# Performance work log

Measured on AMD Instinct MI355X. Metric: run time of the kernel, lower is better.

## Reference

```python
import jax, jax.numpy as jnp
import numpy as np

D_MODEL, H, D_K = 768, 12, 64
B, S = 2, 2048
NEG = -1.0e9


def setup_inputs() -> dict:
    key = jax.random.key(0)
    ks = jax.random.split(key, 7)
    q = jax.random.normal(ks[0], (B, S, D_MODEL), dtype=jnp.float32)
    k = jax.random.normal(ks[1], (B, S, D_MODEL), dtype=jnp.float32)
    v = jax.random.normal(ks[2], (B, S, D_MODEL), dtype=jnp.float32)
    mask = jnp.tril(jnp.ones((S, S), dtype=jnp.int32))[None, None]  # [1,1,S,S] causal
    sc = 1.0 / np.sqrt(D_MODEL)
    w_q = jax.random.normal(ks[3], (D_MODEL, D_MODEL), dtype=jnp.float32) * sc
    w_k = jax.random.normal(ks[4], (D_MODEL, D_MODEL), dtype=jnp.float32) * sc
    w_v = jax.random.normal(ks[5], (D_MODEL, D_MODEL), dtype=jnp.float32) * sc
    w_o = jax.random.normal(ks[6], (D_MODEL, D_MODEL), dtype=jnp.float32) * sc
    return {"q": q, "k": k, "v": v, "mask": mask,
            "w_q": w_q, "w_k": w_k, "w_v": w_v, "w_o": w_o}


def reference(q, k, v, mask, w_q, w_k, w_v, w_o):
    # nn.Linear(x) = x @ W.T ; split heads: [B,S,D] -> [B,H,S,Dk]
    def split_heads(x, w):
        y = jnp.einsum('bsd,ed->bse', x, w)
        return y.reshape(x.shape[0], x.shape[1], H, D_K).transpose(0, 2, 1, 3)

    qh = split_heads(q, w_q)
    kh = split_heads(k, w_k)
    vh = split_heads(v, w_v)
    scores = jnp.einsum('bhqd,bhkd->bhqk', qh, kh) / jnp.sqrt(jnp.float32(D_K))
    scores = jnp.where(mask == 0, jnp.float32(NEG), scores)
    attn = jax.nn.softmax(scores, axis=-1)  # dropout p=0 -> identity
    ctx = jnp.einsum('bhqk,bhkd->bhqd', attn, vh)
    ctx = ctx.transpose(0, 2, 1, 3).reshape(q.shape[0], q.shape[1], D_MODEL)
    return jnp.einsum('bsd,ed->bse', ctx, w_o)
```

## Files before the change

kernel.cpp:

```cpp
#include <hip/hip_runtime.h>

#define DM   768
#define HN   12
#define DKH  64
#define BSZ  2
#define SEQ  2048
#define MROWS (BSZ*SEQ)
#define NEGBIG -1.0e9f

typedef __bf16 bf16;
typedef __bf16 bf16x8 __attribute__((ext_vector_type(8)));
typedef __bf16 bf16x4 __attribute__((ext_vector_type(4)));
typedef float  f32x4  __attribute__((ext_vector_type(4)));
typedef unsigned int uint32;

__device__ __forceinline__ void gload_lds16(const void* g, void* l) {
    __builtin_amdgcn_global_load_lds(
        (const __attribute__((address_space(1))) char*)g,
        (__attribute__((address_space(3))) char*)l, 16, 0, 0);
}

__global__ __launch_bounds__(256) void cvt3(const float* __restrict__ a, const float* __restrict__ b,
                                            const float* __restrict__ c,
                                            bf16* __restrict__ x, bf16* __restrict__ y,
                                            bf16* __restrict__ z, int n) {
    const float* s; bf16* d;
    if      (blockIdx.y == 0) { s = a; d = x; }
    else if (blockIdx.y == 1) { s = b; d = y; }
    else                      { s = c; d = z; }
    int i = (blockIdx.x * 256 + threadIdx.x) * 4;
    if (i + 3 < n) {
        float4 v = *(const float4*)(s + i);
        bf16x4 o; o[0] = (bf16)v.x; o[1] = (bf16)v.y; o[2] = (bf16)v.z; o[3] = (bf16)v.w;
        *(bf16x4*)(d + i) = o;
    }
}
__global__ __launch_bounds__(256) void cvt4(const float* __restrict__ a, const float* __restrict__ b,
                                            const float* __restrict__ c, const float* __restrict__ e,
                                            bf16* __restrict__ x, bf16* __restrict__ y,
                                            bf16* __restrict__ z, bf16* __restrict__ u, int n) {
    const float* s; bf16* d;
    if      (blockIdx.y == 0) { s = a; d = x; }
    else if (blockIdx.y == 1) { s = b; d = y; }
    else if (blockIdx.y == 2) { s = c; d = z; }
    else                      { s = e; d = u; }
    int i = (blockIdx.x * 256 + threadIdx.x) * 4;
    if (i + 3 < n) {
        float4 v = *(const float4*)(s + i);
        bf16x4 o; o[0] = (bf16)v.x; o[1] = (bf16)v.y; o[2] = (bf16)v.z; o[3] = (bf16)v.w;
        *(bf16x4*)(d + i) = o;
    }
}

__global__ __launch_bounds__(256) void gemm_qkv(
    const bf16* __restrict__ xq, const bf16* __restrict__ xk, const bf16* __restrict__ xv,
    const bf16* __restrict__ wq, const bf16* __restrict__ wk, const bf16* __restrict__ wv,
    bf16* __restrict__ qh, bf16* __restrict__ kh, bf16* __restrict__ vt)
{
    __shared__ bf16 As[128 * 32];
    __shared__ bf16 Bs[128 * 32];

    const bf16* A; const bf16* Bw; bf16* Out;
    if      (blockIdx.z == 0) { A = xq; Bw = wq; Out = qh; }
    else if (blockIdx.z == 1) { A = xk; Bw = wk; Out = kh; }
    else                      { A = xv; Bw = wv; Out = vt; }
    const bool vout = (blockIdx.z == 2);

    const int t = threadIdx.x, w = t >> 6, lane = t & 63;
    const int mt = blockIdx.x * 128, nt = blockIdx.y * 128;
    const int wr = (w >> 1) * 64, wc = (w & 1) * 64;

    f32x4 acc[4][4] = {};

    for (int k0 = 0; k0 < DM; k0 += 32) {
        #pragma unroll
        for (int i = 0; i < 2; i++) {
            int c = i * 256 + t;
            int row = c >> 2, col = (c & 3) * 8;
            gload_lds16(A  + (size_t)(mt + row) * DM + k0 + col, (char*)As + c * 16);
            gload_lds16(Bw + (size_t)(nt + row) * DM + k0 + col, (char*)Bs + c * 16);
        }
        asm volatile("s_waitcnt vmcnt(0)" ::: "memory");
        __syncthreads();

        bf16x8 af[4], bfr[4];
        #pragma unroll
        for (int m = 0; m < 4; m++)
            af[m] = *(const bf16x8*)&As[(wr + m * 16 + (lane & 15)) * 32 + (lane >> 4) * 8];
        #pragma unroll
        for (int n = 0; n < 4; n++)
            bfr[n] = *(const bf16x8*)&Bs[(wc + n * 16 + (lane & 15)) * 32 + (lane >> 4) * 8];
        #pragma unroll
        for (int m = 0; m < 4; m++)
            #pragma unroll
            for (int n = 0; n < 4; n++)
                acc[m][n] = __builtin_amdgcn_mfma_f32_16x16x32_bf16(af[m], bfr[n], acc[m][n], 0, 0, 0);
        __syncthreads();
    }

    if (!vout) {
        #pragma unroll
        for (int m = 0; m < 4; m++) {
            #pragma unroll
            for (int n = 0; n < 4; n++) {
                #pragma unroll
                for (int r = 0; r < 4; r++) {
                    int gm = mt + wr + m * 16 + (lane >> 4) * 4 + r;
                    int gn = nt + wc + n * 16 + (lane & 15);
                    int b = gm >> 11, s = gm & 2047, h = gn >> 6, d = gn & 63;
                    Out[(((size_t)b * HN + h) * SEQ + s) * DKH + d] = (bf16)acc[m][n][r];
                }
            }
        }
    } else {
        #pragma unroll
        for (int m = 0; m < 4; m++) {
            #pragma unroll
            for (int n = 0; n < 4; n++) {
                int gm = mt + wr + m * 16 + (lane >> 4) * 4;
                int gn = nt + wc + n * 16 + (lane & 15);
                int b = gm >> 11, s0 = gm & 2047, h = gn >> 6, d = gn & 63;
                bf16x4 pk;
                #pragma unroll
                for (int r = 0; r < 4; r++) pk[r] = (bf16)acc[m][n][r];
                *(bf16x4*)&Out[(((size_t)b * HN + h) * DKH + d) * SEQ + s0] = pk;
            }
        }
    }
}

__global__ __launch_bounds__(256) void gemm_out(
    const bf16* __restrict__ Actx, const bf16* __restrict__ Bw, float* __restrict__ Out)
{
    __shared__ bf16 As[128 * 32];
    __shared__ bf16 Bs[128 * 32];

    const int t = threadIdx.x, w = t >> 6, lane = t & 63;
    const int mt = blockIdx.x * 128, nt = blockIdx.y * 128;
    const int wr = (w >> 1) * 64, wc = (w & 1) * 64;

    f32x4 acc[4][4] = {};

    for (int k0 = 0; k0 < DM; k0 += 32) {
        #pragma unroll
        for (int i = 0; i < 2; i++) {
            int c = i * 256 + t;
            int row = c >> 2, col = (c & 3) * 8;
            gload_lds16(Actx + (size_t)(mt + row) * DM + k0 + col, (char*)As + c * 16);
            gload_lds16(Bw   + (size_t)(nt + row) * DM + k0 + col, (char*)Bs + c * 16);
        }
        asm volatile("s_waitcnt vmcnt(0)" ::: "memory");
        __syncthreads();

        bf16x8 af[4], bfr[4];
        #pragma unroll
        for (int m = 0; m < 4; m++)
            af[m] = *(const bf16x8*)&As[(wr + m * 16 + (lane & 15)) * 32 + (lane >> 4) * 8];
        #pragma unroll
        for (int n = 0; n < 4; n++)
            bfr[n] = *(const bf16x8*)&Bs[(wc + n * 16 + (lane & 15)) * 32 + (lane >> 4) * 8];
        #pragma unroll
        for (int m = 0; m < 4; m++)
            #pragma unroll
            for (int n = 0; n < 4; n++)
                acc[m][n] = __builtin_amdgcn_mfma_f32_16x16x32_bf16(af[m], bfr[n], acc[m][n], 0, 0, 0);
        __syncthreads();
    }

    #pragma unroll
    for (int m = 0; m < 4; m++) {
        #pragma unroll
        for (int n = 0; n < 4; n++) {
            #pragma unroll
            for (int r = 0; r < 4; r++) {
                int gm = mt + wr + m * 16 + (lane >> 4) * 4 + r;
                int gn = nt + wc + n * 16 + (lane & 15);
                Out[(size_t)gm * DM + gn] = acc[m][n][r];
            }
        }
    }
}

__global__ __launch_bounds__(256) void flash_attn(
    const bf16* __restrict__ qh, const bf16* __restrict__ kh,
    const bf16* __restrict__ vt, bf16* __restrict__ ctx)
{
    __shared__ bf16 Ks[2][4096];
    __shared__ bf16 Vs[2][4096];
    __shared__ bf16 pl[4][16 * 72];

    const int qt = (blockIdx.x & 1) ? (31 - (blockIdx.x >> 1)) : (int)(blockIdx.x >> 1);
    const int qb = qt * 64;
    const int bh = blockIdx.y;
    const int t = threadIdx.x, w = t >> 6, lane = t & 63;
    const int g = lane >> 4, lo = lane & 15;
    const size_t base = (size_t)bh * SEQ * DKH;
    const char* khead = (const char*)(kh + base);
    const char* vhead = (const char*)(vt + base);

    uint32 koff[2], voff[2];
    #pragma unroll
    for (int i = 0; i < 2; i++) {
        int c = w * 128 + i * 64 + lane;
        int r = c >> 3, s = c & 7;
        int sw = s ^ (r & 7);
        koff[i] = (uint32)(r * 128  + 16 * sw);
        voff[i] = (uint32)(r * 4096 + 16 * sw);
    }
    const uint32 kr0 = (uint32)(128 * lo + 16 * (g ^ (lo & 7)));
    const uint32 kr1 = kr0 ^ 64;

    const bf16* qp = qh + base + (size_t)(qb + w * 16 + lo) * DKH + g * 8;
    bf16x8 q0 = *(const bf16x8*)qp;
    bf16x8 q1 = *(const bf16x8*)(qp + 32);

    f32x4 O[4] = {};
    float m_old = -1e30f, l_run = 0.0f;
    const int qrow = qb + w * 16 + lo;
    bf16* plw = &pl[w][0];

    const int T = qt + 1;

    #pragma unroll
    for (int i = 0; i < 2; i++) {
        int c16 = (w * 128 + i * 64 + lane) * 16;
        gload_lds16(khead + koff[i], (char*)&Ks[0][0] + c16);
        gload_lds16(vhead + voff[i], (char*)&Vs[0][0] + c16);
    }
    asm volatile("s_waitcnt vmcnt(0)" ::: "memory");
    __syncthreads();

    for (int it = 0; it < T; ++it) {
        const int par = it & 1, nxt = par ^ 1;
        if (it + 1 < T) {
            const char* ks = khead + (size_t)(it + 1) * 8192;
            const char* vs = vhead + (size_t)(it + 1) * 128;
            #pragma unroll
            for (int i = 0; i < 2; i++) {
                int c16 = (w * 128 + i * 64 + lane) * 16;
                gload_lds16(ks + koff[i], (char*)&Ks[nxt][0] + c16);
                gload_lds16(vs + voff[i], (char*)&Vs[nxt][0] + c16);
            }
        }

        const char* Kp = (const char*)&Ks[par][0];
        f32x4 s[4];
        __builtin_amdgcn_s_setprio(1);
        #pragma unroll
        for (int cg = 0; cg < 4; cg++) {
            bf16x8 kf0 = *(const bf16x8*)(Kp + cg * 2048 + kr0);
            bf16x8 kf1 = *(const bf16x8*)(Kp + cg * 2048 + kr1);
            f32x4 z = {0.0f, 0.0f, 0.0f, 0.0f};
            z = __builtin_amdgcn_mfma_f32_16x16x32_bf16(kf0, q0, z, 0, 0, 0);
            z = __builtin_amdgcn_mfma_f32_16x16x32_bf16(kf1, q1, z, 0, 0, 0);
            s[cg] = z;
        }
        __builtin_amdgcn_s_setprio(0);

        if (it == T - 1) {
            #pragma unroll
            for (int cg = 0; cg < 4; cg++)
                #pragma unroll
                for (int r = 0; r < 4; r++) {
                    int ki = it * 64 + cg * 16 + 4 * g + r;
                    float v = s[cg][r] * 0.125f;
                    s[cg][r] = (ki > qrow) ? NEGBIG : v;
                }
        } else {
            #pragma unroll
            for (int cg = 0; cg < 4; cg++)
                #pragma unroll
                for (int r = 0; r < 4; r++) s[cg][r] *= 0.125f;
        }

        float mx = fmaxf(fmaxf(fmaxf(s[0][0], s[0][1]), fmaxf(s[0][2], s[0][3])),
                         fmaxf(fmaxf(s[1][0], s[1][1]), fmaxf(s[1][2], s[1][3])));
        mx = fmaxf(mx, fmaxf(fmaxf(fmaxf(s[2][0], s[2][1]), fmaxf(s[2][2], s[2][3])),
                             fmaxf(fmaxf(s[3][0], s[3][1]), fmaxf(s[3][2], s[3][3]))));
        mx = fmaxf(mx, __shfl_xor(mx, 16, 64));
        mx = fmaxf(mx, __shfl_xor(mx, 32, 64));

        float mnew = fmaxf(m_old, mx);
        float scl  = __expf(m_old - mnew);
        m_old = mnew;
        float rs = 0.0f;
        #pragma unroll
        for (int cg = 0; cg < 4; cg++)
            #pragma unroll
            for (int r = 0; r < 4; r++) {
                s[cg][r] = __expf(s[cg][r] - mnew);
                rs += s[cg][r];
            }
        rs += __shfl_xor(rs, 16, 64);
        rs += __shfl_xor(rs, 32, 64);
        l_run = l_run * scl + rs;

        float scl4[4];
        #pragma unroll
        for (int r = 0; r < 4; r++) scl4[r] = __shfl(scl, 4 * g + r, 64);
        #pragma unroll
        for (int dg = 0; dg < 4; dg++)
            #pragma unroll
            for (int r = 0; r < 4; r++) O[dg][r] *= scl4[r];

        #pragma unroll
        for (int cg = 0; cg < 4; cg++) {
            bf16x4 pk;
            #pragma unroll
            for (int r = 0; r < 4; r++) pk[r] = (bf16)s[cg][r];
            *(bf16x4*)&plw[lo * 72 + cg * 16 + 4 * g] = pk;
        }
        asm volatile("s_waitcnt lgkmcnt(0)" ::: "memory");
        __builtin_amdgcn_sched_barrier(0);

        const char* Vp = (const char*)&Vs[par][0];
        __builtin_amdgcn_s_setprio(1);
        #pragma unroll
        for (int kq = 0; kq < 2; kq++) {
            bf16x8 pa = *(const bf16x8*)&plw[lo * 72 + kq * 32 + 8 * g];
            #pragma unroll
            for (int dblk = 0; dblk < 4; dblk++) {
                int row = dblk * 16 + lo;
                bf16x8 vv = *(const bf16x8*)(Vp + row * 128 + 16 * ((4 * kq + g) ^ (lo & 7)));
                O[dblk] = __builtin_amdgcn_mfma_f32_16x16x32_bf16(pa, vv, O[dblk], 0, 0, 0);
            }
        }
        __builtin_amdgcn_s_setprio(0);

        asm volatile("s_waitcnt vmcnt(0)" ::: "memory");
        __syncthreads();
    }

    float inv4[4];
    #pragma unroll
    for (int r = 0; r < 4; r++) inv4[r] = 1.0f / __shfl(l_run, 4 * g + r, 64);
    const int b = bh / HN, h = bh % HN;
    #pragma unroll
    for (int dg = 0; dg < 4; dg++) {
        #pragma unroll
        for (int r = 0; r < 4; r++) {
            int row = qb + w * 16 + g * 4 + r;
            ctx[((size_t)(b * SEQ + row)) * DM + h * DKH + dg * 16 + lo] =
                (bf16)(O[dg][r] * inv4[r]);
        }
    }
}

extern "C" void kernel_launch(void* const* d_in, const int* in_sizes, int n_in,
                              void* d_out, int out_size, void* d_ws, size_t ws_size,
                              hipStream_t stream) {
    const float* q  = (const float*)d_in[0];
    const float* k  = (const float*)d_in[1];
    const float* v  = (const float*)d_in[2];
    const float* wq = (const float*)d_in[4];
    const float* wk = (const float*)d_in[5];
    const float* wv = (const float*)d_in[6];
    const float* wo = (const float*)d_in[7];
    float* out = (float*)d_out;

    const size_t NX = (size_t)MROWS * DM;
    const size_t NW = (size_t)DM * DM;

    bf16* p = (bf16*)d_ws;
    bf16* xq  = p; p += NX;
    bf16* xk  = p; p += NX;
    bf16* xv  = p; p += NX;
    bf16* wqb = p; p += NW;
    bf16* wkb = p; p += NW;
    bf16* wvb = p; p += NW;
    bf16* wob = p; p += NW;
    bf16* qhp = p; p += NX;
    bf16* khp = p; p += NX;
    bf16* vtp = p; p += NX;
    bf16* ctxp = p; p += NX;

    cvt3<<<dim3(NX / 1024, 3), 256, 0, stream>>>(q, k, v, xq, xk, xv, (int)NX);
    cvt4<<<dim3(NW / 1024, 4), 256, 0, stream>>>(wq, wk, wv, wo, wqb, wkb, wvb, wob, (int)NW);

    gemm_qkv<<<dim3(MROWS / 128, DM / 128, 3), 256, 0, stream>>>(
        xq, xk, xv, wqb, wkb, wvb, qhp, khp, vtp);

    flash_attn<<<dim3(SEQ / 64, BSZ * HN), 256, 0, stream>>>(qhp, khp, vtp, ctxp);

    gemm_out<<<dim3(MROWS / 128, DM / 128), 256, 0, stream>>>(ctxp, wob, out);
}
```

Before: 120.1 us.

## Process two query tiles per attention block and skip rescaling when max barely changes

Each flash-attention block now handles 128 query rows (two 64-row halves per wave group), so every K/V tile loaded into LDS is reused for twice as many queries. The grid becomes 1D, with the longest causal tiles scheduled first, and launch bounds now request 3 blocks per CU. Online softmax skips the O/l rescale unless the running max rises by more than 8, which cuts exp and multiply work. The cost is higher register pressure from two accumulators and fewer, longer blocks, which may hurt load balance.

```diff
diff --git a/kernel.cpp b/kernel.cpp
--- a/kernel.cpp
+++ b/kernel.cpp
@@ -181,17 +181,18 @@
     }
 }
 
-__global__ __launch_bounds__(256) void flash_attn(
+__global__ __launch_bounds__(256, 3) void flash_attn(
     const bf16* __restrict__ qh, const bf16* __restrict__ kh,
     const bf16* __restrict__ vt, bf16* __restrict__ ctx)
 {
     __shared__ bf16 Ks[2][4096];
     __shared__ bf16 Vs[2][4096];
-    __shared__ bf16 pl[4][16 * 72];
-
-    const int qt = (blockIdx.x & 1) ? (31 - (blockIdx.x >> 1)) : (int)(blockIdx.x >> 1);
-    const int qb = qt * 64;
-    const int bh = blockIdx.y;
+    __shared__ bf16 pl[4][32 * 72];
+
+    const int bid = blockIdx.x;
+    const int qt = 15 - bid / 24;
+    const int bh = bid % 24;
+    const int qb = qt * 128;
     const int t = threadIdx.x, w = t >> 6, lane = t & 63;
     const int g = lane >> 4, lo = lane & 15;
     const size_t base = (size_t)bh * SEQ * DKH;
@@ -210,16 +211,20 @@
     const uint32 kr0 = (uint32)(128 * lo + 16 * (g ^ (lo & 7)));
     const uint32 kr1 = kr0 ^ 64;
 
-    const bf16* qp = qh + base + (size_t)(qb + w * 16 + lo) * DKH + g * 8;
-    bf16x8 q0 = *(const bf16x8*)qp;
-    bf16x8 q1 = *(const bf16x8*)(qp + 32);
-
-    f32x4 O[4] = {};
-    float m_old = -1e30f, l_run = 0.0f;
-    const int qrow = qb + w * 16 + lo;
+    const int qrow0 = qb + 16 * w + lo;
+    const int qrow1 = qb + 64 + 16 * w + lo;
+    const bf16* qp0 = qh + base + (size_t)qrow0 * DKH + g * 8;
+    const bf16* qp1 = qh + base + (size_t)qrow1 * DKH + g * 8;
+    bf16x8 qa0 = *(const bf16x8*)qp0;
+    bf16x8 qa1 = *(const bf16x8*)(qp0 + 32);
+    bf16x8 qb0 = *(const bf16x8*)qp1;
+    bf16x8 qb1 = *(const bf16x8*)(qp1 + 32);
+
+    f32x4 O0[4] = {}, O1[4] = {};
+    float m0 = -1e30f, l0 = 0.0f, m1 = -1e30f, l1 = 0.0f;
     bf16* plw = &pl[w][0];
 
-    const int T = qt + 1;
+    const int T = 2 * qt + 2;
 
     #pragma unroll
     for (int i = 0; i < 2; i++) {
@@ -243,105 +248,199 @@
             }
         }
 
+        const bool act0  = (it != T - 1);
+        const bool diag0 = (it == T - 2);
+        const bool diag1 = (it == T - 1);
+
         const char* Kp = (const char*)&Ks[par][0];
-        f32x4 s[4];
-        __builtin_amdgcn_s_setprio(1);
-        #pragma unroll
-        for (int cg = 0; cg < 4; cg++) {
-            bf16x8 kf0 = *(const bf16x8*)(Kp + cg * 2048 + kr0);
-            bf16x8 kf1 = *(const bf16x8*)(Kp + cg * 2048 + kr1);
-            f32x4 z = {0.0f, 0.0f, 0.0f, 0.0f};
-            z = __builtin_amdgcn_mfma_f32_16x16x32_bf16(kf0, q0, z, 0, 0, 0);
-            z = __builtin_amdgcn_mfma_f32_16x16x32_bf16(kf1, q1, z, 0, 0, 0);
-            s[cg] = z;
-        }
-        __builtin_amdgcn_s_setprio(0);
-
-        if (it == T - 1) {
+        f32x4 s0[4], s1[4];
+        {
+            bf16x8 kf0[4], kf1[4];
+            #pragma unroll
+            for (int cg = 0; cg < 4; cg++) {
+                kf0[cg] = *(const bf16x8*)(Kp + cg * 2048 + kr0);
+                kf1[cg] = *(const bf16x8*)(Kp + cg * 2048 + kr1);
+            }
+            __builtin_amdgcn_s_setprio(1);
+            if (act0) {
+                #pragma unroll
+                for (int cg = 0; cg < 4; cg++) {
+                    f32x4 z = {0.0f, 0.0f, 0.0f, 0.0f};
+                    z = __builtin_amdgcn_mfma_f32_16x16x32_bf16(kf0[cg], qa0, z, 0, 0, 0);
+                    z = __builtin_amdgcn_mfma_f32_16x16x32_bf16(kf1[cg], qa1, z, 0, 0, 0);
+                    s0[cg] = z;
+                }
+            }
+            #pragma unroll
+            for (int cg = 0; cg < 4; cg++) {
+                f32x4 z = {0.0f, 0.0f, 0.0f, 0.0f};
+                z = __builtin_amdgcn_mfma_f32_16x16x32_bf16(kf0[cg], qb0, z, 0, 0, 0);
+                z = __builtin_amdgcn_mfma_f32_16x16x32_bf16(kf1[cg], qb1, z, 0, 0, 0);
+                s1[cg] = z;
+            }
+            __builtin_amdgcn_s_setprio(0);
+        }
+
+        if (act0) {
+            if (diag0) {
+                #pragma unroll
+                for (int cg = 0; cg < 4; cg++)
+                    #pragma unroll
+                    for (int r = 0; r < 4; r++) {
+                        int ki = it * 64 + cg * 16 + 4 * g + r;
+                        float v = s0[cg][r] * 0.125f;
+                        s0[cg][r] = (ki > qrow0) ? NEGBIG : v;
+                    }
+            } else {
+                #pragma unroll
+                for (int cg = 0; cg < 4; cg++)
+                    #pragma unroll
+                    for (int r = 0; r < 4; r++) s0[cg][r] *= 0.125f;
+            }
+        }
+        if (diag1) {
             #pragma unroll
             for (int cg = 0; cg < 4; cg++)
                 #pragma unroll
                 for (int r = 0; r < 4; r++) {
                     int ki = it * 64 + cg * 16 + 4 * g + r;
-                    float v = s[cg][r] * 0.125f;
-                    s[cg][r] = (ki > qrow) ? NEGBIG : v;
+                    float v = s1[cg][r] * 0.125f;
+                    s1[cg][r] = (ki > qrow1) ? NEGBIG : v;
                 }
         } else {
             #pragma unroll
             for (int cg = 0; cg < 4; cg++)
                 #pragma unroll
-                for (int r = 0; r < 4; r++) s[cg][r] *= 0.125f;
-        }
-
-        float mx = fmaxf(fmaxf(fmaxf(s[0][0], s[0][1]), fmaxf(s[0][2], s[0][3])),
-                         fmaxf(fmaxf(s[1][0], s[1][1]), fmaxf(s[1][2], s[1][3])));
-        mx = fmaxf(mx, fmaxf(fmaxf(fmaxf(s[2][0], s[2][1]), fmaxf(s[2][2], s[2][3])),
-                             fmaxf(fmaxf(s[3][0], s[3][1]), fmaxf(s[3][2], s[3][3]))));
-        mx = fmaxf(mx, __shfl_xor(mx, 16, 64));
-        mx = fmaxf(mx, __shfl_xor(mx, 32, 64));
-
-        float mnew = fmaxf(m_old, mx);
-        float scl  = __expf(m_old - mnew);
-        m_old = mnew;
-        float rs = 0.0f;
-        #pragma unroll
-        for (int cg = 0; cg < 4; cg++)
-            #pragma unroll
-            for (int r = 0; r < 4; r++) {
-                s[cg][r] = __expf(s[cg][r] - mnew);
-                rs += s[cg][r];
-            }
-        rs += __shfl_xor(rs, 16, 64);
-        rs += __shfl_xor(rs, 32, 64);
-        l_run = l_run * scl + rs;
-
-        float scl4[4];
-        #pragma unroll
-        for (int r = 0; r < 4; r++) scl4[r] = __shfl(scl, 4 * g + r, 64);
-        #pragma unroll
-        for (int dg = 0; dg < 4; dg++)
-            #pragma unroll
-            for (int r = 0; r < 4; r++) O[dg][r] *= scl4[r];
-
-        #pragma unroll
-        for (int cg = 0; cg < 4; cg++) {
-            bf16x4 pk;
-            #pragma unroll
-            for (int r = 0; r < 4; r++) pk[r] = (bf16)s[cg][r];
-            *(bf16x4*)&plw[lo * 72 + cg * 16 + 4 * g] = pk;
-        }
-        asm volatile("s_waitcnt lgkmcnt(0)" ::: "memory");
-        __builtin_amdgcn_sched_barrier(0);
-
-        const char* Vp = (const char*)&Vs[par][0];
-        __builtin_amdgcn_s_setprio(1);
-        #pragma unroll
-        for (int kq = 0; kq < 2; kq++) {
-            bf16x8 pa = *(const bf16x8*)&plw[lo * 72 + kq * 32 + 8 * g];
-            #pragma unroll
-            for (int dblk = 0; dblk < 4; dblk++) {
-                int row = dblk * 16 + lo;
-                bf16x8 vv = *(const bf16x8*)(Vp + row * 128 + 16 * ((4 * kq + g) ^ (lo & 7)));
-                O[dblk] = __builtin_amdgcn_mfma_f32_16x16x32_bf16(pa, vv, O[dblk], 0, 0, 0);
-            }
-        }
-        __builtin_amdgcn_s_setprio(0);
+                for (int r = 0; r < 4; r++) s1[cg][r] *= 0.125f;
+        }
+
+        if (act0) {
+            float mx = fmaxf(fmaxf(fmaxf(s0[0][0], s0[0][1]), fmaxf(s0[0][2], s0[0][3])),
+                             fmaxf(fmaxf(s0[1][0], s0[1][1]), fmaxf(s0[1][2], s0[1][3])));
+            mx = fmaxf(mx, fmaxf(fmaxf(fmaxf(s0[2][0], s0[2][1]), fmaxf(s0[2][2], s0[2][3])),
+                                 fmaxf(fmaxf(s0[3][0], s0[3][1]), fmaxf(s0[3][2], s0[3][3]))));
+            mx = fmaxf(mx, __shfl_xor(mx, 16, 64));
+            mx = fmaxf(mx, __shfl_xor(mx, 32, 64));
+            if (!__all(mx - m0 <= 8.0f)) {
+                float mnew = fmaxf(m0, mx);
+                float scl = __expf(m0 - mnew);
+                m0 = mnew; l0 *= scl;
+                float s4[4];
+                #pragma unroll
+                for (int r = 0; r < 4; r++) s4[r] = __shfl(scl, 4 * g + r, 64);
+                #pragma unroll
+                for (int dg = 0; dg < 4; dg++)
+                    #pragma unroll
+                    for (int r = 0; r < 4; r++) O0[dg][r] *= s4[r];
+            }
+            float rs = 0.0f;
+            #pragma unroll
+            for (int cg = 0; cg < 4; cg++)
+                #pragma unroll
+                for (int r = 0; r < 4; r++) {
+                    s0[cg][r] = __expf(s0[cg][r] - m0);
+                    rs += s0[cg][r];
+                }
+            rs += __shfl_xor(rs, 16, 64);
+            rs += __shfl_xor(rs, 32, 64);
+            l0 += rs;
+            #pragma unroll
+            for (int cg = 0; cg < 4; cg++) {
+                bf16x4 pk;
+                #pragma unroll
+                for (int r = 0; r < 4; r++) pk[r] = (bf16)s0[cg][r];
+                *(bf16x4*)&plw[lo * 72 + cg * 16 + 4 * g] = pk;
+            }
+        }
+        {
+            float mx = fmaxf(fmaxf(fmaxf(s1[0][0], s1[0][1]), fmaxf(s1[0][2], s1[0][3])),
+                             fmaxf(fmaxf(s1[1][0], s1[1][1]), fmaxf(s1[1][2], s1[1][3])));
+            mx = fmaxf(mx, fmaxf(fmaxf(fmaxf(s1[2][0], s1[2][1]), fmaxf(s1[2][2], s1[2][3])),
+                                 fmaxf(fmaxf(s1[3][0], s1[3][1]), fmaxf(s1[3][2], s1[3][3]))));
+            mx = fmaxf(mx, __shfl_xor(mx, 16, 64));
+            mx = fmaxf(mx, __shfl_xor(mx, 32, 64));
+            if (!__all(mx - m1 <= 8.0f)) {
+                float mnew = fmaxf(m1, mx);
+                float scl = __expf(m1 - mnew);
+                m1 = mnew; l1 *= scl;
+                float s4[4];
+                #pragma unroll
+                for (int r = 0; r < 4; r++) s4[r] = __shfl(scl, 4 * g + r, 64);
+                #pragma unroll
+                for (int dg = 0; dg < 4; dg++)
+                    #pragma unroll
+                    for (int r = 0; r < 4; r++) O1[dg][r] *= s4[r];
+            }
+            float rs = 0.0f;
+            #pragma unroll
+            for (int cg = 0; cg < 4; cg++)
+                #pragma unroll
+                for (int r = 0; r < 4; r++) {
+                    s1[cg][r] = __expf(s1[cg][r] - m1);
+                    rs += s1[cg][r];
+                }
+            rs += __shfl_xor(rs, 16, 64);
+            rs += __shfl_xor(rs, 32, 64);
+            l1 += rs;
+            #pragma unroll
+            for (int cg = 0; cg < 4; cg++) {
+                bf16x4 pk;
+                #pragma unroll
+                for (int r = 0; r < 4; r++) pk[r] = (bf16)s1[cg][r];
+                *(bf16x4*)&plw[(16 + lo) * 72 + cg * 16 + 4 * g] = pk;
+            }
+        }
+
+        {
+            const char* Vp = (const char*)&Vs[par][0];
+            bf16x8 vv[8];
+            #pragma unroll
+            for (int kq = 0; kq < 2; kq++)
+                #pragma unroll
+                for (int dblk = 0; dblk < 4; dblk++)
+                    vv[kq * 4 + dblk] = *(const bf16x8*)
+                        (Vp + (dblk * 16 + lo) * 128 + 16 * ((4 * kq + g) ^ (lo & 7)));
+            __builtin_amdgcn_s_setprio(1);
+            if (act0) {
+                #pragma unroll
+                for (int kq = 0; kq < 2; kq++) {
+                    bf16x8 pa = *(const bf16x8*)&plw[lo * 72 + kq * 32 + 8 * g];
+                    #pragma unroll
+                    for (int dblk = 0; dblk < 4; dblk++)
+                        O0[dblk] = __builtin_amdgcn_mfma_f32_16x16x32_bf16(pa, vv[kq * 4 + dblk], O0[dblk], 0, 0, 0);
+                }
+            }
+            #pragma unroll
+            for (int kq = 0; kq < 2; kq++) {
+                bf16x8 pa = *(const bf16x8*)&plw[(16 + lo) * 72 + kq * 32 + 8 * g];
+                #pragma unroll
+                for (int dblk = 0; dblk < 4; dblk++)
+                    O1[dblk] = __builtin_amdgcn_mfma_f32_16x16x32_bf16(pa, vv[kq * 4 + dblk], O1[dblk], 0, 0, 0);
+            }
+            __builtin_amdgcn_s_setprio(0);
+        }
 
         asm volatile("s_waitcnt vmcnt(0)" ::: "memory");
         __syncthreads();
     }
 
-    float inv4[4];
+    const int b = bh / HN, h = bh % HN;
+    float inv0[4], inv1[4];
     #pragma unroll
-    for (int r = 0; r < 4; r++) inv4[r] = 1.0f / __shfl(l_run, 4 * g + r, 64);
-    const int b = bh / HN, h = bh % HN;
+    for (int r = 0; r < 4; r++) {
+        inv0[r] = 1.0f / __shfl(l0, 4 * g + r, 64);
+        inv1[r] = 1.0f / __shfl(l1, 4 * g + r, 64);
+    }
     #pragma unroll
     for (int dg = 0; dg < 4; dg++) {
         #pragma unroll
         for (int r = 0; r < 4; r++) {
-            int row = qb + w * 16 + g * 4 + r;
-            ctx[((size_t)(b * SEQ + row)) * DM + h * DKH + dg * 16 + lo] =
-                (bf16)(O[dg][r] * inv4[r]);
+            int row0 = qb + 16 * w + g * 4 + r;
+            int row1 = qb + 64 + 16 * w + g * 4 + r;
+            ctx[((size_t)(b * SEQ + row0)) * DM + h * DKH + dg * 16 + lo] =
+                (bf16)(O0[dg][r] * inv0[r]);
+            ctx[((size_t)(b * SEQ + row1)) * DM + h * DKH + dg * 16 + lo] =
+                (bf16)(O1[dg][r] * inv1[r]);
         }
     }
 }
@@ -380,7 +479,7 @@
     gemm_qkv<<<dim3(MROWS / 128, DM / 128, 3), 256, 0, stream>>>(
         xq, xk, xv, wqb, wkb, wvb, qhp, khp, vtp);
 
-    flash_attn<<<dim3(SEQ / 64, BSZ * HN), 256, 0, stream>>>(qhp, khp, vtp, ctxp);
+    flash_attn<<<(SEQ / 128) * (BSZ * HN), 256, 0, stream>>>(qhp, khp, vtp, ctxp);
 
     gemm_out<<<dim3(MROWS / 128, DM / 128), 256, 0, stream>>>(ctxp, wob, out);
 }
```

New measurement: 121.6 us. No clear change (+1.3%).
